# Optimization experiments

Measured on AMD Instinct MI355X. Metric: run time of the kernel, lower is better.

## Reference

```python
import jax, jax.numpy as jnp
import numpy as np

HIDDEN = 1024


def setup_inputs() -> dict:
    key = jax.random.key(0)
    ks = jax.random.split(key, 9)
    B, S, Kq, H = 16, 4096, 64, HIDDEN
    scale = 1.0 / np.sqrt(H)
    return {
        "queries": jax.random.normal(ks[0], (B, Kq, H), jnp.float32),
        "keys": jax.random.normal(ks[1], (B, S, H), jnp.float32),
        "values": jax.random.normal(ks[2], (B, S, H), jnp.float32),
        "Wq": jax.random.normal(ks[3], (H, H), jnp.float32) * scale,
        "bq": jax.random.normal(ks[4], (H,), jnp.float32) * 0.02,
        "Wk": jax.random.normal(ks[5], (H, H), jnp.float32) * scale,
        "bk": jax.random.normal(ks[6], (H,), jnp.float32) * 0.02,
        "Wv": jax.random.normal(ks[7], (H, H), jnp.float32) * scale,
        "bv": jax.random.normal(ks[8], (H,), jnp.float32) * 0.02,
    }


def reference(queries, keys, values, Wq, bq, Wk, bk, Wv, bv):
    H = Wq.shape[0]
    scaling = jax.lax.rsqrt(jnp.asarray(H, queries.dtype))
    # torch Linear: x @ W^T + b
    q = queries @ Wq.T + bq            # (B, Kq, H)
    k = keys @ Wk.T + bk               # (B, S, H)
    v = values @ Wv.T + bv             # (B, S, H)
    # scores: k @ q^T -> (B, S, Kq), softmax over seq_len axis (dim=1)
    scores = jnp.einsum('bsh,bqh->bsq', k, q) * scaling
    attention_weights = jax.nn.softmax(scores, axis=1)
    # context: attn^T @ v -> (B, Kq, H)
    context = jnp.einsum('bsq,bsh->bqh', attention_weights, v)
    return context, attention_weights
```

## Files before the change

kernel.cpp:

```cpp
#include <hip/hip_runtime.h>
#include <hip/hip_bf16.h>

#define H 1024
#define SEQ 4096
#define BQ 64
#define NB 16

typedef float f32x4 __attribute__((ext_vector_type(4)));
typedef __bf16 bf16x8 __attribute__((ext_vector_type(8)));

__device__ __forceinline__ void split_bf16(const float* x, bf16x8& hi, bf16x8& lo)
{
    #pragma unroll
    for (int i = 0; i < 8; ++i) {
        float v = x[i];
        __bf16 h = (__bf16)v;
        hi[i] = h;
        lo[i] = (__bf16)(v - (float)h);
    }
}

__device__ __forceinline__ void gload_lds16(const float* g, void* lds)
{
    __builtin_amdgcn_global_load_lds(
        (const __attribute__((address_space(1))) void*)g,
        (__attribute__((address_space(3))) void*)lds, 16, 0, 0);
}

__global__ __launch_bounds__(256)
void mfma_gemm_bt(const float* __restrict__ A, const float* __restrict__ Bm,
                  const float* __restrict__ bias, float* __restrict__ C, float scale)
{
    const int m0 = blockIdx.x * 64;
    const int n0 = blockIdx.y * 64;
    const int w   = threadIdx.x >> 6;
    const int l   = threadIdx.x & 63;
    const int row = l & 15;
    const int kg  = l >> 4;

    const float* ap = A + (size_t)(m0 + w * 16 + row) * H + kg * 8;
    const float* bp = Bm + (size_t)(n0 + row) * H + kg * 8;

    f32x4 acc[4] = {};
    for (int k0 = 0; k0 < H; k0 += 32) {
        float a8[8];
        *reinterpret_cast<float4*>(&a8[0]) = *reinterpret_cast<const float4*>(ap + k0);
        *reinterpret_cast<float4*>(&a8[4]) = *reinterpret_cast<const float4*>(ap + k0 + 4);
        bf16x8 ahi, alo;
        split_bf16(a8, ahi, alo);
        #pragma unroll
        for (int j = 0; j < 4; ++j) {
            float b8[8];
            const float* bjp = bp + (size_t)j * 16 * H + k0;
            *reinterpret_cast<float4*>(&b8[0]) = *reinterpret_cast<const float4*>(bjp);
            *reinterpret_cast<float4*>(&b8[4]) = *reinterpret_cast<const float4*>(bjp + 4);
            bf16x8 bhi, blo;
            split_bf16(b8, bhi, blo);
            acc[j] = __builtin_amdgcn_mfma_f32_16x16x32_bf16(ahi, bhi, acc[j], 0, 0, 0);
            acc[j] = __builtin_amdgcn_mfma_f32_16x16x32_bf16(ahi, blo, acc[j], 0, 0, 0);
            acc[j] = __builtin_amdgcn_mfma_f32_16x16x32_bf16(alo, bhi, acc[j], 0, 0, 0);
        }
    }
    #pragma unroll
    for (int j = 0; j < 4; ++j) {
        int n = n0 + j * 16 + row;
        float bb = bias ? bias[n] : 0.f;
        #pragma unroll
        for (int r = 0; r < 4; ++r) {
            int m = m0 + w * 16 + kg * 4 + r;
            C[(size_t)m * H + n] = acc[j][r] * scale + bb;
        }
    }
}

__global__ __launch_bounds__(256)
void transpose_k(const float* __restrict__ Wk, float* __restrict__ WkT)
{
    __shared__ float tile[64][65];
    const int k0 = blockIdx.x * 64;
    const int n0 = blockIdx.y * 64;
    const int t  = threadIdx.x;
    const int c4 = (t & 15) * 4;
    const int r  = t >> 4;
    #pragma unroll
    for (int p = 0; p < 4; ++p) {
        float4 v = *reinterpret_cast<const float4*>(&Wk[(size_t)(k0 + r + 16 * p) * H + n0 + c4]);
        tile[r + 16 * p][c4 + 0] = v.x;
        tile[r + 16 * p][c4 + 1] = v.y;
        tile[r + 16 * p][c4 + 2] = v.z;
        tile[r + 16 * p][c4 + 3] = v.w;
    }
    __syncthreads();
    #pragma unroll
    for (int p = 0; p < 4; ++p) {
        int rr = r + 16 * p;
        float4 o;
        o.x = tile[c4 + 0][rr];
        o.y = tile[c4 + 1][rr];
        o.z = tile[c4 + 2][rr];
        o.w = tile[c4 + 3][rr];
        *reinterpret_cast<float4*>(&WkT[(size_t)(n0 + rr) * H + k0 + c4]) = o;
    }
}

__global__ __launch_bounds__(256)
void ngemm_bt(const float* __restrict__ A, const float* __restrict__ Bm,
              __bf16* __restrict__ Nhi, __bf16* __restrict__ Nlo, float scale)
{
    const int m0 = blockIdx.x * 64;
    const int n0 = blockIdx.y * 64;
    const int w   = threadIdx.x >> 6;
    const int l   = threadIdx.x & 63;
    const int row = l & 15;
    const int kg  = l >> 4;

    const float* ap = A + (size_t)(m0 + w * 16 + row) * H + kg * 8;
    const float* bp = Bm + (size_t)(n0 + row) * H + kg * 8;

    f32x4 acc[4] = {};
    for (int k0 = 0; k0 < H; k0 += 32) {
        float a8[8];
        *reinterpret_cast<float4*>(&a8[0]) = *reinterpret_cast<const float4*>(ap + k0);
        *reinterpret_cast<float4*>(&a8[4]) = *reinterpret_cast<const float4*>(ap + k0 + 4);
        bf16x8 ahi, alo;
        split_bf16(a8, ahi, alo);
        #pragma unroll
        for (int j = 0; j < 4; ++j) {
            float b8[8];
            const float* bjp = bp + (size_t)j * 16 * H + k0;
            *reinterpret_cast<float4*>(&b8[0]) = *reinterpret_cast<const float4*>(bjp);
            *reinterpret_cast<float4*>(&b8[4]) = *reinterpret_cast<const float4*>(bjp + 4);
            bf16x8 bhi, blo;
            split_bf16(b8, bhi, blo);
            acc[j] = __builtin_amdgcn_mfma_f32_16x16x32_bf16(ahi, bhi, acc[j], 0, 0, 0);
            acc[j] = __builtin_amdgcn_mfma_f32_16x16x32_bf16(ahi, blo, acc[j], 0, 0, 0);
            acc[j] = __builtin_amdgcn_mfma_f32_16x16x32_bf16(alo, bhi, acc[j], 0, 0, 0);
        }
    }
    #pragma unroll
    for (int j = 0; j < 4; ++j) {
        int n = n0 + j * 16 + row;
        #pragma unroll
        for (int r = 0; r < 4; ++r) {
            int m = m0 + w * 16 + kg * 4 + r;
            float v = acc[j][r] * scale;
            __bf16 hi = (__bf16)v;
            Nhi[(size_t)m * H + n] = hi;
            Nlo[(size_t)m * H + n] = (__bf16)(v - (float)hi);
        }
    }
}

__global__ __launch_bounds__(256)
void cvec_kernel(const float* __restrict__ q, const float* __restrict__ bk,
                 float* __restrict__ cvec, float scale)
{
    int r = blockIdx.x * 4 + (threadIdx.x >> 6);
    int l = threadIdx.x & 63;
    float s = 0.f;
    #pragma unroll
    for (int i = 0; i < 16; ++i)
        s += q[(size_t)r * H + l + 64 * i] * bk[l + 64 * i];
    #pragma unroll
    for (int off = 32; off; off >>= 1)
        s += __shfl_down(s, off);
    if (l == 0) cvec[r] = s * scale;
}

__global__ __launch_bounds__(512)
void scores_mfma(const float* __restrict__ keys,
                 const __bf16* __restrict__ Nhi, const __bf16* __restrict__ Nlo,
                 const float* __restrict__ cvec, float* __restrict__ scores)
{
    const int id = blockIdx.x;
    const int x  = id & 7;
    const int m  = id >> 3;
    const int b  = 2 * x + (m >> 5);
    const int s0 = (m & 31) * 128;

    const int t   = threadIdx.x;
    const int w   = t >> 6;
    const int l   = t & 63;
    const int row = l & 15;
    const int kg  = l >> 4;

    __shared__ __bf16 nshH[64][16][8];
    __shared__ __bf16 nshL[64][16][8];

    const float* ka = keys + ((size_t)b * SEQ + s0 + w * 16 + row) * H + kg * 8;
    const __bf16* nhb = Nhi + (size_t)b * BQ * H;
    const __bf16* nlb = Nlo + (size_t)b * BQ * H;

    const int sqi = (t >> 4) & 31;
    const int skb = t & 15;

    f32x4 acc[4] = {};
    for (int c = 0; c < 8; ++c) {
        const int kc = c * 128;
        float4 kr[8];
        #pragma unroll
        for (int ii = 0; ii < 4; ++ii) {
            kr[2 * ii + 0] = *reinterpret_cast<const float4*>(ka + kc + ii * 32);
            kr[2 * ii + 1] = *reinterpret_cast<const float4*>(ka + kc + ii * 32 + 4);
        }
        bf16x8 nh[2], nl[2];
        #pragma unroll
        for (int rep = 0; rep < 2; ++rep) {
            size_t go = (size_t)(rep * 32 + sqi) * H + kc + skb * 8;
            nh[rep] = *reinterpret_cast<const bf16x8*>(nhb + go);
            nl[rep] = *reinterpret_cast<const bf16x8*>(nlb + go);
        }
        __syncthreads();
        #pragma unroll
        for (int rep = 0; rep < 2; ++rep) {
            *reinterpret_cast<bf16x8*>(&nshH[rep * 32 + sqi][skb][0]) = nh[rep];
            *reinterpret_cast<bf16x8*>(&nshL[rep * 32 + sqi][skb][0]) = nl[rep];
        }
        __syncthreads();
        #pragma unroll
        for (int ii = 0; ii < 4; ++ii) {
            float a8[8];
            *reinterpret_cast<float4*>(&a8[0]) = kr[2 * ii + 0];
            *reinterpret_cast<float4*>(&a8[4]) = kr[2 * ii + 1];
            bf16x8 ahi, alo;
            split_bf16(a8, ahi, alo);
            const int kb = ii * 4 + kg;
            #pragma unroll
            for (int j = 0; j < 4; ++j) {
                const int qi = j * 16 + row;
                bf16x8 bhi = *reinterpret_cast<const bf16x8*>(&nshH[qi][kb][0]);
                bf16x8 blo = *reinterpret_cast<const bf16x8*>(&nshL[qi][kb][0]);
                acc[j] = __builtin_amdgcn_mfma_f32_16x16x32_bf16(ahi, bhi, acc[j], 0, 0, 0);
                acc[j] = __builtin_amdgcn_mfma_f32_16x16x32_bf16(ahi, blo, acc[j], 0, 0, 0);
                acc[j] = __builtin_amdgcn_mfma_f32_16x16x32_bf16(alo, bhi, acc[j], 0, 0, 0);
            }
        }
    }
    #pragma unroll
    for (int j = 0; j < 4; ++j) {
        int qi = j * 16 + row;
        float cv = cvec[b * BQ + qi];
        #pragma unroll
        for (int r = 0; r < 4; ++r) {
            int s = s0 + w * 16 + kg * 4 + r;
            scores[((size_t)b * SEQ + s) * BQ + qi] = acc[j][r] + cv;
        }
    }
}

__global__ __launch_bounds__(256)
void sm_partial(const float* __restrict__ scores, float* __restrict__ pmax,
                float* __restrict__ psum)
{
    const int b  = blockIdx.y;
    const int ch = blockIdx.x;
    const int t  = threadIdx.x;
    const int qi = t & 63;
    const int g  = t >> 6;
    const float* sb = scores + ((size_t)b * SEQ + ch * 128) * BQ;
    float v[32];
    #pragma unroll
    for (int i = 0; i < 32; ++i)
        v[i] = sb[(size_t)(g + i * 4) * BQ + qi];
    float m = v[0];
    #pragma unroll
    for (int i = 1; i < 32; ++i) m = fmaxf(m, v[i]);
    __shared__ float red[4][64];
    red[g][qi] = m;
    __syncthreads();
    float M = fmaxf(fmaxf(red[0][qi], red[1][qi]), fmaxf(red[2][qi], red[3][qi]));
    float sum = 0.f;
    #pragma unroll
    for (int i = 0; i < 32; ++i) sum += __expf(v[i] - M);
    __syncthreads();
    red[g][qi] = sum;
    __syncthreads();
    if (g == 0) {
        float ssum = red[0][qi] + red[1][qi] + red[2][qi] + red[3][qi];
        pmax[((size_t)b * 32 + ch) * 64 + qi] = M;
        psum[((size_t)b * 32 + ch) * 64 + qi] = ssum;
    }
}

__global__ void sm_combine(const float* __restrict__ pmax,
                           const float* __restrict__ psum,
                           float* __restrict__ gstat)
{
    int b  = blockIdx.x;
    int qi = threadIdx.x;
    float m = -1e30f;
    for (int c = 0; c < 32; ++c)
        m = fmaxf(m, pmax[((size_t)b * 32 + c) * 64 + qi]);
    float s = 0.f;
    for (int c = 0; c < 32; ++c)
        s += psum[((size_t)b * 32 + c) * 64 + qi] *
             __expf(pmax[((size_t)b * 32 + c) * 64 + qi] - m);
    gstat[(size_t)b * 64 + qi] = m;
    gstat[(size_t)(NB + b) * 64 + qi] = 1.f / s;
}

__global__ __launch_bounds__(256)
void sm_norm(float* __restrict__ attn, const float* __restrict__ gstat,
             __hip_bfloat16* __restrict__ abfT)
{
    __shared__ float tile[64][133];
    const int b  = blockIdx.y;
    const int ch = blockIdx.x;
    const int t  = threadIdx.x;
    const int qi = t & 63;
    const int g  = t >> 6;
    const float M   = gstat[(size_t)b * 64 + qi];
    const float inv = gstat[(size_t)(NB + b) * 64 + qi];
    float* sb = attn + ((size_t)b * SEQ + ch * 128) * BQ;
    #pragma unroll 8
    for (int i = 0; i < 32; ++i) {
        int sl = g + i * 4;
        size_t idx = (size_t)sl * BQ + qi;
        float w = __expf(sb[idx] - M) * inv;
        sb[idx] = w;
        tile[qi][sl] = w;
    }
    __syncthreads();
    const int qo = t >> 2;
    const int c  = (t & 3) * 32;
    __hip_bfloat16* dst = abfT + ((size_t)(b * BQ + qo)) * SEQ + ch * 128 + c;
    #pragma unroll
    for (int v = 0; v < 4; ++v) {
        bf16x8 w8;
        #pragma unroll
        for (int e = 0; e < 8; ++e)
            w8[e] = (__bf16)tile[qo][c + v * 8 + e];
        *reinterpret_cast<bf16x8*>(dst + v * 8) = w8;
    }
}

template<int SC>
__global__ __launch_bounds__(256)
void tmat_mfma(const __hip_bfloat16* __restrict__ abfT,
               const float* __restrict__ values,
               float* __restrict__ Tpart)
{
    const int i  = blockIdx.x;
    const int h0 = ((i >> 3) & 7) * 128;
    const int g  = (i & 7) + 8 * (i >> 6);
    const int b  = g / SC;
    const int sc = g % SC;
    const int schunk = SEQ / SC;

    const int w   = threadIdx.x >> 6;
    const int l   = threadIdx.x & 63;
    const int row = l & 15;
    const int kg  = l >> 4;
    const int sbase = sc * schunk;

    __shared__ float vlds[2][32][128];

    const __hip_bfloat16* ap = abfT + ((size_t)b * BQ + row) * SEQ + sbase + kg * 8;
    const float* vb = values + ((size_t)b * SEQ + sbase) * H + h0;

    const int nk = schunk / 32;

    #define STAGE(buf, k0)                                                     \
        {                                                                      \
            _Pragma("unroll")                                                  \
            for (int ii = 0; ii < 4; ++ii) {                                   \
                int elem = w * 1024 + ii * 256 + l * 4;                        \
                int k    = elem >> 7;                                          \
                int cc   = elem & 127;                                         \
                int csw  = cc ^ ((k >> 3) << 4);                               \
                const float* src = vb + (size_t)((k0) + k) * H + csw;          \
                gload_lds16(src, (void*)(&vlds[buf][0][0] + w * 1024 + ii * 256)); \
            }                                                                  \
        }

    f32x4 acc[4][2] = {};
    STAGE(0, 0);
    __syncthreads();

    for (int ks = 0; ks < nk; ++ks) {
        const int buf = ks & 1;
        if (ks + 1 < nk) STAGE(buf ^ 1, (ks + 1) * 32);
        const int k0 = ks * 32;
        bf16x8 a[4];
        #pragma unroll
        for (int q = 0; q < 4; ++q)
            a[q] = *reinterpret_cast<const bf16x8*>(ap + (size_t)q * 16 * SEQ + k0);
        #pragma unroll
        for (int j = 0; j < 2; ++j) {
            const int col = (w * 32 + j * 16 + row) ^ (kg << 4);
            float b8[8];
            #pragma unroll
            for (int e = 0; e < 8; ++e)
                b8[e] = vlds[buf][kg * 8 + e][col];
            bf16x8 bhi, blo;
            split_bf16(b8, bhi, blo);
            #pragma unroll
            for (int q = 0; q < 4; ++q) {
                acc[q][j] = __builtin_amdgcn_mfma_f32_16x16x32_bf16(a[q], bhi, acc[q][j], 0, 0, 0);
                acc[q][j] = __builtin_amdgcn_mfma_f32_16x16x32_bf16(a[q], blo, acc[q][j], 0, 0, 0);
            }
        }
        __syncthreads();
    }
    #undef STAGE

    float* tp = Tpart + ((size_t)sc * NB + b) * BQ * H;
    #pragma unroll
    for (int q = 0; q < 4; ++q) {
        #pragma unroll
        for (int j = 0; j < 2; ++j) {
            int h = h0 + w * 32 + j * 16 + row;
            #pragma unroll
            for (int r = 0; r < 4; ++r) {
                int qi = q * 16 + kg * 4 + r;
                tp[(size_t)qi * H + h] = acc[q][j][r];
            }
        }
    }
}

template<int SC>
__global__ __launch_bounds__(256)
void tsum_kernel(float* __restrict__ Tpart)
{
    const size_t stride = (size_t)NB * BQ * H;
    size_t i = ((size_t)blockIdx.x * 256 + threadIdx.x) * 4;
    f32x4 s = *reinterpret_cast<const f32x4*>(Tpart + i);
    #pragma unroll
    for (int p = 1; p < SC; ++p)
        s += *reinterpret_cast<const f32x4*>(Tpart + p * stride + i);
    *reinterpret_cast<f32x4*>(Tpart + i) = s;
}

extern "C" void kernel_launch(void* const* d_in, const int* in_sizes, int n_in,
                              void* d_out, int out_size, void* d_ws, size_t ws_size,
                              hipStream_t stream)
{
    const float* queries = (const float*)d_in[0];
    const float* keys    = (const float*)d_in[1];
    const float* values  = (const float*)d_in[2];
    const float* Wq = (const float*)d_in[3];
    const float* bq = (const float*)d_in[4];
    const float* Wk = (const float*)d_in[5];
    const float* bk = (const float*)d_in[6];
    const float* Wv = (const float*)d_in[7];
    const float* bv = (const float*)d_in[8];

    float* out     = (float*)d_out;
    float* context = out;
    float* attn    = out + (size_t)NB * BQ * H;

    const int SC = (ws_size >= (41ull << 20)) ? 8 : 2;

    char* ws = (char*)d_ws;
    float* q     = (float*)ws;
    float* WkT   = (float*)(ws + (4ull << 20));
    __bf16* Nhi  = (__bf16*)(ws + (8ull << 20));
    __bf16* Nlo  = (__bf16*)(ws + (10ull << 20));
    float* Tpart = (float*)ws;
    __hip_bfloat16* abfT = (__hip_bfloat16*)(ws + (size_t)SC * (4ull << 20));
    char* smalls = ws + (size_t)SC * (4ull << 20) + (8ull << 20);
    float* cvec  = (float*)smalls;
    float* gstat = (float*)(smalls + (64u << 10));
    float* pmax  = (float*)(smalls + (128u << 10));
    float* psum  = (float*)(smalls + (512u << 10));

    const float scale = 0.03125f;

    transpose_k<<<dim3(16, 16), 256, 0, stream>>>(Wk, WkT);
    mfma_gemm_bt<<<dim3(16, 16), 256, 0, stream>>>(queries, Wq, bq, q, 1.0f);
    ngemm_bt<<<dim3(16, 16), 256, 0, stream>>>(q, WkT, Nhi, Nlo, scale);
    cvec_kernel<<<256, 256, 0, stream>>>(q, bk, cvec, scale);
    scores_mfma<<<512, 512, 0, stream>>>(keys, Nhi, Nlo, cvec, attn);
    sm_partial<<<dim3(32, NB), 256, 0, stream>>>(attn, pmax, psum);
    sm_combine<<<NB, 64, 0, stream>>>(pmax, psum, gstat);
    sm_norm<<<dim3(32, NB), 256, 0, stream>>>(attn, gstat, abfT);
    if (SC == 8) tmat_mfma<8><<<8 * NB * 8, 256, 0, stream>>>(abfT, values, Tpart);
    else         tmat_mfma<2><<<8 * NB * 2, 256, 0, stream>>>(abfT, values, Tpart);
    if (SC == 8) tsum_kernel<8><<<1024, 256, 0, stream>>>(Tpart);
    else         tsum_kernel<2><<<1024, 256, 0, stream>>>(Tpart);
    mfma_gemm_bt<<<dim3(16, 16), 256, 0, stream>>>(Tpart, Wv, bv, context, 1.0f);
}
```

Measured before the change: 294.2 us.

## Split-K the small GEMMs and double-buffer a smaller-tile scores kernel

The three 1024x1024x1024 projection GEMMs become split-K launches with four K slices (1024 blocks instead of 256), each followed by a combine kernel that sums the partials and applies bias, scale or the bf16 hi/lo split. The scores kernel moves to 64-row tiles with 256 threads and 1024 blocks. It double-buffers LDS and registers across sixteen 64-wide K chunks with one barrier per chunk and XOR-swizzles the LDS layout to avoid bank conflicts. The softmax partial pass is regridded to match the 64 chunks. The aim is to fill more CUs and hide load latency, at the cost of extra partial-sum traffic and more kernel launches.

Measured after the change: 323.3 us. +9.9%, slower.

```diff
diff --git a/kernel.cpp b/kernel.cpp
--- a/kernel.cpp
+++ b/kernel.cpp
@@ -74,51 +74,22 @@
 }
 
 __global__ __launch_bounds__(256)
-void transpose_k(const float* __restrict__ Wk, float* __restrict__ WkT)
-{
-    __shared__ float tile[64][65];
-    const int k0 = blockIdx.x * 64;
-    const int n0 = blockIdx.y * 64;
-    const int t  = threadIdx.x;
-    const int c4 = (t & 15) * 4;
-    const int r  = t >> 4;
-    #pragma unroll
-    for (int p = 0; p < 4; ++p) {
-        float4 v = *reinterpret_cast<const float4*>(&Wk[(size_t)(k0 + r + 16 * p) * H + n0 + c4]);
-        tile[r + 16 * p][c4 + 0] = v.x;
-        tile[r + 16 * p][c4 + 1] = v.y;
-        tile[r + 16 * p][c4 + 2] = v.z;
-        tile[r + 16 * p][c4 + 3] = v.w;
-    }
-    __syncthreads();
-    #pragma unroll
-    for (int p = 0; p < 4; ++p) {
-        int rr = r + 16 * p;
-        float4 o;
-        o.x = tile[c4 + 0][rr];
-        o.y = tile[c4 + 1][rr];
-        o.z = tile[c4 + 2][rr];
-        o.w = tile[c4 + 3][rr];
-        *reinterpret_cast<float4*>(&WkT[(size_t)(n0 + rr) * H + k0 + c4]) = o;
-    }
-}
-
-__global__ __launch_bounds__(256)
-void ngemm_bt(const float* __restrict__ A, const float* __restrict__ Bm,
-              __bf16* __restrict__ Nhi, __bf16* __restrict__ Nlo, float scale)
+void mfma_gemm_sk(const float* __restrict__ A, const float* __restrict__ Bm,
+                  float* __restrict__ P)
 {
     const int m0 = blockIdx.x * 64;
     const int n0 = blockIdx.y * 64;
+    const int kb = blockIdx.z * 256;
     const int w   = threadIdx.x >> 6;
     const int l   = threadIdx.x & 63;
     const int row = l & 15;
     const int kg  = l >> 4;
 
-    const float* ap = A + (size_t)(m0 + w * 16 + row) * H + kg * 8;
-    const float* bp = Bm + (size_t)(n0 + row) * H + kg * 8;
+    const float* ap = A + (size_t)(m0 + w * 16 + row) * H + kb + kg * 8;
+    const float* bp = Bm + (size_t)(n0 + row) * H + kb + kg * 8;
 
     f32x4 acc[4] = {};
-    for (int k0 = 0; k0 < H; k0 += 32) {
+    for (int k0 = 0; k0 < 256; k0 += 32) {
         float a8[8];
         *reinterpret_cast<float4*>(&a8[0]) = *reinterpret_cast<const float4*>(ap + k0);
         *reinterpret_cast<float4*>(&a8[4]) = *reinterpret_cast<const float4*>(ap + k0 + 4);
@@ -137,6 +108,110 @@
             acc[j] = __builtin_amdgcn_mfma_f32_16x16x32_bf16(alo, bhi, acc[j], 0, 0, 0);
         }
     }
+    float* pp = P + ((size_t)blockIdx.z << 20);
+    #pragma unroll
+    for (int j = 0; j < 4; ++j) {
+        int n = n0 + j * 16 + row;
+        #pragma unroll
+        for (int r = 0; r < 4; ++r) {
+            int m = m0 + w * 16 + kg * 4 + r;
+            pp[(size_t)m * H + n] = acc[j][r];
+        }
+    }
+}
+
+template<int MODE>
+__global__ __launch_bounds__(256)
+void combine4(const float* __restrict__ P, const float* __restrict__ bias,
+              float* __restrict__ C, __bf16* __restrict__ Chi,
+              __bf16* __restrict__ Clo, float scale)
+{
+    size_t i = ((size_t)blockIdx.x * 256 + threadIdx.x) * 4;
+    f32x4 s = *reinterpret_cast<const f32x4*>(P + i);
+    s += *reinterpret_cast<const f32x4*>(P + (1u << 20) + i);
+    s += *reinterpret_cast<const f32x4*>(P + (2u << 20) + i);
+    s += *reinterpret_cast<const f32x4*>(P + (3u << 20) + i);
+    if (MODE == 0) {
+        f32x4 bb = *reinterpret_cast<const f32x4*>(bias + (i & 1023));
+        f32x4 o;
+        #pragma unroll
+        for (int j = 0; j < 4; ++j) o[j] = s[j] * scale + bb[j];
+        *reinterpret_cast<f32x4*>(C + i) = o;
+    } else {
+        #pragma unroll
+        for (int j = 0; j < 4; ++j) {
+            float v = s[j] * scale;
+            __bf16 h = (__bf16)v;
+            Chi[i + j] = h;
+            Clo[i + j] = (__bf16)(v - (float)h);
+        }
+    }
+}
+
+__global__ __launch_bounds__(256)
+void transpose_k(const float* __restrict__ Wk, float* __restrict__ WkT)
+{
+    __shared__ float tile[64][65];
+    const int k0 = blockIdx.x * 64;
+    const int n0 = blockIdx.y * 64;
+    const int t  = threadIdx.x;
+    const int c4 = (t & 15) * 4;
+    const int r  = t >> 4;
+    #pragma unroll
+    for (int p = 0; p < 4; ++p) {
+        float4 v = *reinterpret_cast<const float4*>(&Wk[(size_t)(k0 + r + 16 * p) * H + n0 + c4]);
+        tile[r + 16 * p][c4 + 0] = v.x;
+        tile[r + 16 * p][c4 + 1] = v.y;
+        tile[r + 16 * p][c4 + 2] = v.z;
+        tile[r + 16 * p][c4 + 3] = v.w;
+    }
+    __syncthreads();
+    #pragma unroll
+    for (int p = 0; p < 4; ++p) {
+        int rr = r + 16 * p;
+        float4 o;
+        o.x = tile[c4 + 0][rr];
+        o.y = tile[c4 + 1][rr];
+        o.z = tile[c4 + 2][rr];
+        o.w = tile[c4 + 3][rr];
+        *reinterpret_cast<float4*>(&WkT[(size_t)(n0 + rr) * H + k0 + c4]) = o;
+    }
+}
+
+__global__ __launch_bounds__(256)
+void ngemm_bt(const float* __restrict__ A, const float* __restrict__ Bm,
+              __bf16* __restrict__ Nhi, __bf16* __restrict__ Nlo, float scale)
+{
+    const int m0 = blockIdx.x * 64;
+    const int n0 = blockIdx.y * 64;
+    const int w   = threadIdx.x >> 6;
+    const int l   = threadIdx.x & 63;
+    const int row = l & 15;
+    const int kg  = l >> 4;
+
+    const float* ap = A + (size_t)(m0 + w * 16 + row) * H + kg * 8;
+    const float* bp = Bm + (size_t)(n0 + row) * H + kg * 8;
+
+    f32x4 acc[4] = {};
+    for (int k0 = 0; k0 < H; k0 += 32) {
+        float a8[8];
+        *reinterpret_cast<float4*>(&a8[0]) = *reinterpret_cast<const float4*>(ap + k0);
+        *reinterpret_cast<float4*>(&a8[4]) = *reinterpret_cast<const float4*>(ap + k0 + 4);
+        bf16x8 ahi, alo;
+        split_bf16(a8, ahi, alo);
+        #pragma unroll
+        for (int j = 0; j < 4; ++j) {
+            float b8[8];
+            const float* bjp = bp + (size_t)j * 16 * H + k0;
+            *reinterpret_cast<float4*>(&b8[0]) = *reinterpret_cast<const float4*>(bjp);
+            *reinterpret_cast<float4*>(&b8[4]) = *reinterpret_cast<const float4*>(bjp + 4);
+            bf16x8 bhi, blo;
+            split_bf16(b8, bhi, blo);
+            acc[j] = __builtin_amdgcn_mfma_f32_16x16x32_bf16(ahi, bhi, acc[j], 0, 0, 0);
+            acc[j] = __builtin_amdgcn_mfma_f32_16x16x32_bf16(ahi, blo, acc[j], 0, 0, 0);
+            acc[j] = __builtin_amdgcn_mfma_f32_16x16x32_bf16(alo, bhi, acc[j], 0, 0, 0);
+        }
+    }
     #pragma unroll
     for (int j = 0; j < 4; ++j) {
         int n = n0 + j * 16 + row;
@@ -167,7 +242,7 @@
     if (l == 0) cvec[r] = s * scale;
 }
 
-__global__ __launch_bounds__(512)
+__global__ __launch_bounds__(256)
 void scores_mfma(const float* __restrict__ keys,
                  const __bf16* __restrict__ Nhi, const __bf16* __restrict__ Nlo,
                  const float* __restrict__ cvec, float* __restrict__ scores)
@@ -175,8 +250,8 @@
     const int id = blockIdx.x;
     const int x  = id & 7;
     const int m  = id >> 3;
-    const int b  = 2 * x + (m >> 5);
-    const int s0 = (m & 31) * 128;
+    const int b  = 2 * x + (m >> 6);
+    const int s0 = (m & 63) * 64;
 
     const int t   = threadIdx.x;
     const int w   = t >> 6;
@@ -184,58 +259,77 @@
     const int row = l & 15;
     const int kg  = l >> 4;
 
-    __shared__ __bf16 nshH[64][16][8];
-    __shared__ __bf16 nshL[64][16][8];
+    __shared__ __bf16 nshH[2][64][8][8];
+    __shared__ __bf16 nshL[2][64][8][8];
 
     const float* ka = keys + ((size_t)b * SEQ + s0 + w * 16 + row) * H + kg * 8;
     const __bf16* nhb = Nhi + (size_t)b * BQ * H;
     const __bf16* nlb = Nlo + (size_t)b * BQ * H;
 
-    const int sqi = (t >> 4) & 31;
-    const int skb = t & 15;
+    const int sqi  = t >> 2;
+    const int skb0 = (t & 3) * 2;
+    const int ws0  = (skb0 + 0) ^ (sqi & 7);
+    const int ws1  = (skb0 + 1) ^ (sqi & 7);
+
+    float4 kr[2][4];
+    bf16x8 nh[2][2], nl[2][2];
+
+    #pragma unroll
+    for (int ii = 0; ii < 2; ++ii) {
+        kr[0][2 * ii + 0] = *reinterpret_cast<const float4*>(ka + ii * 32);
+        kr[0][2 * ii + 1] = *reinterpret_cast<const float4*>(ka + ii * 32 + 4);
+    }
+    #pragma unroll
+    for (int u = 0; u < 2; ++u) {
+        size_t go = (size_t)sqi * H + (skb0 + u) * 8;
+        nh[0][u] = *reinterpret_cast<const bf16x8*>(nhb + go);
+        nl[0][u] = *reinterpret_cast<const bf16x8*>(nlb + go);
+    }
 
     f32x4 acc[4] = {};
-    for (int c = 0; c < 8; ++c) {
-        const int kc = c * 128;
-        float4 kr[8];
-        #pragma unroll
-        for (int ii = 0; ii < 4; ++ii) {
-            kr[2 * ii + 0] = *reinterpret_cast<const float4*>(ka + kc + ii * 32);
-            kr[2 * ii + 1] = *reinterpret_cast<const float4*>(ka + kc + ii * 32 + 4);
-        }
-        bf16x8 nh[2], nl[2];
-        #pragma unroll
-        for (int rep = 0; rep < 2; ++rep) {
-            size_t go = (size_t)(rep * 32 + sqi) * H + kc + skb * 8;
-            nh[rep] = *reinterpret_cast<const bf16x8*>(nhb + go);
-            nl[rep] = *reinterpret_cast<const bf16x8*>(nlb + go);
-        }
+    #pragma unroll
+    for (int c = 0; c < 16; ++c) {
+        const int buf = c & 1;
+        *reinterpret_cast<bf16x8*>(&nshH[buf][sqi][ws0][0]) = nh[buf][0];
+        *reinterpret_cast<bf16x8*>(&nshH[buf][sqi][ws1][0]) = nh[buf][1];
+        *reinterpret_cast<bf16x8*>(&nshL[buf][sqi][ws0][0]) = nl[buf][0];
+        *reinterpret_cast<bf16x8*>(&nshL[buf][sqi][ws1][0]) = nl[buf][1];
         __syncthreads();
-        #pragma unroll
-        for (int rep = 0; rep < 2; ++rep) {
-            *reinterpret_cast<bf16x8*>(&nshH[rep * 32 + sqi][skb][0]) = nh[rep];
-            *reinterpret_cast<bf16x8*>(&nshL[rep * 32 + sqi][skb][0]) = nl[rep];
-        }
-        __syncthreads();
-        #pragma unroll
-        for (int ii = 0; ii < 4; ++ii) {
+        if (c < 15) {
+            const int kc = (c + 1) * 64;
+            #pragma unroll
+            for (int ii = 0; ii < 2; ++ii) {
+                kr[buf ^ 1][2 * ii + 0] = *reinterpret_cast<const float4*>(ka + kc + ii * 32);
+                kr[buf ^ 1][2 * ii + 1] = *reinterpret_cast<const float4*>(ka + kc + ii * 32 + 4);
+            }
+            #pragma unroll
+            for (int u = 0; u < 2; ++u) {
+                size_t go = (size_t)sqi * H + kc + (skb0 + u) * 8;
+                nh[buf ^ 1][u] = *reinterpret_cast<const bf16x8*>(nhb + go);
+                nl[buf ^ 1][u] = *reinterpret_cast<const bf16x8*>(nlb + go);
+            }
+        }
+        #pragma unroll
+        for (int ii = 0; ii < 2; ++ii) {
             float a8[8];
-            *reinterpret_cast<float4*>(&a8[0]) = kr[2 * ii + 0];
-            *reinterpret_cast<float4*>(&a8[4]) = kr[2 * ii + 1];
+            *reinterpret_cast<float4*>(&a8[0]) = kr[buf][2 * ii + 0];
+            *reinterpret_cast<float4*>(&a8[4]) = kr[buf][2 * ii + 1];
             bf16x8 ahi, alo;
             split_bf16(a8, ahi, alo);
             const int kb = ii * 4 + kg;
+            const int slot = kb ^ (row & 7);
             #pragma unroll
             for (int j = 0; j < 4; ++j) {
                 const int qi = j * 16 + row;
-                bf16x8 bhi = *reinterpret_cast<const bf16x8*>(&nshH[qi][kb][0]);
-                bf16x8 blo = *reinterpret_cast<const bf16x8*>(&nshL[qi][kb][0]);
+                bf16x8 bhi = *reinterpret_cast<const bf16x8*>(&nshH[buf][qi][slot][0]);
+                bf16x8 blo = *reinterpret_cast<const bf16x8*>(&nshL[buf][qi][slot][0]);
                 acc[j] = __builtin_amdgcn_mfma_f32_16x16x32_bf16(ahi, bhi, acc[j], 0, 0, 0);
                 acc[j] = __builtin_amdgcn_mfma_f32_16x16x32_bf16(ahi, blo, acc[j], 0, 0, 0);
                 acc[j] = __builtin_amdgcn_mfma_f32_16x16x32_bf16(alo, bhi, acc[j], 0, 0, 0);
             }
         }
     }
+
     #pragma unroll
     for (int j = 0; j < 4; ++j) {
         int qi = j * 16 + row;
@@ -257,28 +351,28 @@
     const int t  = threadIdx.x;
     const int qi = t & 63;
     const int g  = t >> 6;
-    const float* sb = scores + ((size_t)b * SEQ + ch * 128) * BQ;
-    float v[32];
-    #pragma unroll
-    for (int i = 0; i < 32; ++i)
+    const float* sb = scores + ((size_t)b * SEQ + ch * 64) * BQ;
+    float v[16];
+    #pragma unroll
+    for (int i = 0; i < 16; ++i)
         v[i] = sb[(size_t)(g + i * 4) * BQ + qi];
     float m = v[0];
     #pragma unroll
-    for (int i = 1; i < 32; ++i) m = fmaxf(m, v[i]);
+    for (int i = 1; i < 16; ++i) m = fmaxf(m, v[i]);
     __shared__ float red[4][64];
     red[g][qi] = m;
     __syncthreads();
     float M = fmaxf(fmaxf(red[0][qi], red[1][qi]), fmaxf(red[2][qi], red[3][qi]));
     float sum = 0.f;
     #pragma unroll
-    for (int i = 0; i < 32; ++i) sum += __expf(v[i] - M);
+    for (int i = 0; i < 16; ++i) sum += __expf(v[i] - M);
     __syncthreads();
     red[g][qi] = sum;
     __syncthreads();
     if (g == 0) {
         float ssum = red[0][qi] + red[1][qi] + red[2][qi] + red[3][qi];
-        pmax[((size_t)b * 32 + ch) * 64 + qi] = M;
-        psum[((size_t)b * 32 + ch) * 64 + qi] = ssum;
+        pmax[((size_t)b * 64 + ch) * 64 + qi] = M;
+        psum[((size_t)b * 64 + ch) * 64 + qi] = ssum;
     }
 }
 
@@ -289,12 +383,12 @@
     int b  = blockIdx.x;
     int qi = threadIdx.x;
     float m = -1e30f;
-    for (int c = 0; c < 32; ++c)
-        m = fmaxf(m, pmax[((size_t)b * 32 + c) * 64 + qi]);
+    for (int c = 0; c < 64; ++c)
+        m = fmaxf(m, pmax[((size_t)b * 64 + c) * 64 + qi]);
     float s = 0.f;
-    for (int c = 0; c < 32; ++c)
-        s += psum[((size_t)b * 32 + c) * 64 + qi] *
-             __expf(pmax[((size_t)b * 32 + c) * 64 + qi] - m);
+    for (int c = 0; c < 64; ++c)
+        s += psum[((size_t)b * 64 + c) * 64 + qi] *
+             __expf(pmax[((size_t)b * 64 + c) * 64 + qi] - m);
     gstat[(size_t)b * 64 + qi] = m;
     gstat[(size_t)(NB + b) * 64 + qi] = 1.f / s;
 }
@@ -450,34 +544,49 @@
     float* context = out;
     float* attn    = out + (size_t)NB * BQ * H;
 
-    const int SC = (ws_size >= (41ull << 20)) ? 8 : 2;
+    const bool BIG = (ws_size >= (41ull << 20));
+    const int SC = BIG ? 8 : 2;
 
     char* ws = (char*)d_ws;
     float* q     = (float*)ws;
     float* WkT   = (float*)(ws + (4ull << 20));
     __bf16* Nhi  = (__bf16*)(ws + (8ull << 20));
     __bf16* Nlo  = (__bf16*)(ws + (10ull << 20));
+    float* GP1   = (float*)(ws + (12ull << 20));
+    float* GP2   = (float*)(ws + (4ull << 20));
     float* Tpart = (float*)ws;
     __hip_bfloat16* abfT = (__hip_bfloat16*)(ws + (size_t)SC * (4ull << 20));
     char* smalls = ws + (size_t)SC * (4ull << 20) + (8ull << 20);
     float* cvec  = (float*)smalls;
     float* gstat = (float*)(smalls + (64u << 10));
     float* pmax  = (float*)(smalls + (128u << 10));
-    float* psum  = (float*)(smalls + (512u << 10));
+    float* psum  = (float*)(smalls + (384u << 10));
 
     const float scale = 0.03125f;
 
     transpose_k<<<dim3(16, 16), 256, 0, stream>>>(Wk, WkT);
-    mfma_gemm_bt<<<dim3(16, 16), 256, 0, stream>>>(queries, Wq, bq, q, 1.0f);
-    ngemm_bt<<<dim3(16, 16), 256, 0, stream>>>(q, WkT, Nhi, Nlo, scale);
+    if (BIG) {
+        mfma_gemm_sk<<<dim3(16, 16, 4), 256, 0, stream>>>(queries, Wq, GP1);
+        combine4<0><<<1024, 256, 0, stream>>>(GP1, bq, q, nullptr, nullptr, 1.0f);
+        mfma_gemm_sk<<<dim3(16, 16, 4), 256, 0, stream>>>(q, WkT, GP1);
+        combine4<1><<<1024, 256, 0, stream>>>(GP1, nullptr, nullptr, Nhi, Nlo, scale);
+    } else {
+        mfma_gemm_bt<<<dim3(16, 16), 256, 0, stream>>>(queries, Wq, bq, q, 1.0f);
+        ngemm_bt<<<dim3(16, 16), 256, 0, stream>>>(q, WkT, Nhi, Nlo, scale);
+    }
     cvec_kernel<<<256, 256, 0, stream>>>(q, bk, cvec, scale);
-    scores_mfma<<<512, 512, 0, stream>>>(keys, Nhi, Nlo, cvec, attn);
-    sm_partial<<<dim3(32, NB), 256, 0, stream>>>(attn, pmax, psum);
+    scores_mfma<<<1024, 256, 0, stream>>>(keys, Nhi, Nlo, cvec, attn);
+    sm_partial<<<dim3(64, NB), 256, 0, stream>>>(attn, pmax, psum);
     sm_combine<<<NB, 64, 0, stream>>>(pmax, psum, gstat);
     sm_norm<<<dim3(32, NB), 256, 0, stream>>>(attn, gstat, abfT);
     if (SC == 8) tmat_mfma<8><<<8 * NB * 8, 256, 0, stream>>>(abfT, values, Tpart);
     else         tmat_mfma<2><<<8 * NB * 2, 256, 0, stream>>>(abfT, values, Tpart);
     if (SC == 8) tsum_kernel<8><<<1024, 256, 0, stream>>>(Tpart);
     else         tsum_kernel<2><<<1024, 256, 0, stream>>>(Tpart);
-    mfma_gemm_bt<<<dim3(16, 16), 256, 0, stream>>>(Tpart, Wv, bv, context, 1.0f);
-}
+    if (BIG) {
+        mfma_gemm_sk<<<dim3(16, 16, 4), 256, 0, stream>>>(Tpart, Wv, GP2);
+        combine4<0><<<1024, 256, 0, stream>>>(GP2, bv, context, nullptr, nullptr, 1.0f);
+    } else {
+        mfma_gemm_bt<<<dim3(16, 16), 256, 0, stream>>>(Tpart, Wv, bv, context, 1.0f);
+    }
+}
```
